# Performance work log

Measured on AMD Instinct MI355X. Metric: run time of the kernel, lower is better.

Reference implementation:

```python
import jax, jax.numpy as jnp
import numpy as np

B, T_DEC, S_ENC, D = 4, 128, 1024, 512
UNITS = 128


def setup_inputs() -> dict:
    key = jax.random.key(0)
    ks = jax.random.split(key, 5)
    dec = jax.random.normal(ks[0], (B, T_DEC, D), dtype=jnp.float32)
    enc = jax.random.normal(ks[1], (B, S_ENC, D), dtype=jnp.float32)
    # Glorot-ish scaled dense params
    W1 = jax.random.normal(ks[2], (D, UNITS), dtype=jnp.float32) / np.sqrt(D)
    b1 = jnp.zeros((UNITS,), dtype=jnp.float32)
    W2 = jax.random.normal(ks[3], (D, UNITS), dtype=jnp.float32) / np.sqrt(D)
    b2 = jnp.zeros((UNITS,), dtype=jnp.float32)
    v = jax.random.normal(ks[4], (UNITS,), dtype=jnp.float32) / np.sqrt(UNITS)
    v_b = jnp.zeros((1,), dtype=jnp.float32)
    return {"decoder_output": dec, "encoder_output": enc,
            "W1": W1, "b1": b1, "W2": W2, "b2": b2, "v": v, "v_b": v_b}


def reference(decoder_output, encoder_output, W1, b1, W2, b2, v, v_b):
    # Hoist the loop-invariant encoder projection (original recomputes it per step).
    w_enc = encoder_output @ W1 + b1            # [B, S, U]
    w_dec = decoder_output @ W2 + b2            # [B, T, U]
    # score[b,t,s] = v . tanh(w_enc[b,s] + w_dec[b,t]) + v_bias
    feat = jnp.tanh(w_enc[:, None, :, :] + w_dec[:, :, None, :])  # [B, T, S, U]
    scores = jnp.einsum('btsu,u->bts', feat, v) + v_b[0]          # [B, T, S]
    attention_weights = jax.nn.softmax(scores, axis=-1)           # [B, T, S]
    context_vector = jnp.einsum('bts,bsd->btd', attention_weights, encoder_output)
    return (context_vector, attention_weights)
```

## Files before the change

kernel.cpp:

```cpp
#include <hip/hip_runtime.h>
#include <math.h>

#define NB 4
#define TD 128
#define SE 1024
#define DD 512
#define UN 128
#define KSPLIT 4
#define SSPLIT 8

__device__ __forceinline__ float exp2_raw(float x) {
  float r;
  asm("v_exp_f32 %0, %1" : "=v"(r) : "v"(x));
  return r;
}

__global__ __launch_bounds__(512, 2) void k_proj(const float* __restrict__ enc,
                                                 const float* __restrict__ dec,
                                                 const float* __restrict__ W1,
                                                 const float* __restrict__ b1,
                                                 const float* __restrict__ W2,
                                                 const float* __restrict__ b2,
                                                 float* __restrict__ wencT,
                                                 float* __restrict__ wdec) {
  __shared__ __align__(16) float At[16 * DD];
  __shared__ float red[KSPLIT][16][129];

  const int tx = threadIdx.x;
  const int rb = blockIdx.x;
  const bool is_enc = rb < 256;
  const int row_base = rb * 16;
  const float* __restrict__ src = is_enc
      ? (enc + (size_t)row_base * DD)
      : (dec + (size_t)(row_base - NB * SE) * DD);
  const float* __restrict__ W = is_enc ? W1 : W2;
  const float* __restrict__ bias = is_enc ? b1 : b2;
  const float K2 = 2.88539008f;

#pragma unroll
  for (int i = 0; i < 4; ++i) {
    const int idx = (i * 512 + tx) * 4;
    *(float4*)&At[idx] = *(const float4*)(src + idx);
  }
  __syncthreads();

  const int u2 = (tx & 63) * 2;
  const int wave = tx >> 6;
  const int ks = wave & 3;
  const int rh = wave >> 2;
  const int kb = ks * 128;
  const float* __restrict__ Wp = W + (size_t)kb * UN + u2;

  float acc[8][2] = {};
  for (int k = 0; k < 128; k += 4) {
    float4 a[8];
#pragma unroll
    for (int r = 0; r < 8; ++r)
      a[r] = *(const float4*)&At[(rh * 8 + r) * DD + kb + k];
#pragma unroll
    for (int j = 0; j < 4; ++j) {
      const float2 w = *(const float2*)(Wp + (size_t)(k + j) * UN);
#pragma unroll
      for (int r = 0; r < 8; ++r) {
        const float arj = ((const float*)&a[r])[j];
        acc[r][0] = fmaf(arj, w.x, acc[r][0]);
        acc[r][1] = fmaf(arj, w.y, acc[r][1]);
      }
    }
  }

#pragma unroll
  for (int r = 0; r < 8; ++r) {
    red[ks][rh * 8 + r][u2]     = acc[r][0];
    red[ks][rh * 8 + r][u2 + 1] = acc[r][1];
  }
  __syncthreads();

  const int u = tx >> 2;
  const int rq = (tx & 3) * 4;
  const float bu = bias[u];
  float o[4];
#pragma unroll
  for (int j = 0; j < 4; ++j) {
    const int row = rq + j;
    const float s = (red[0][row][u] + red[1][row][u]) +
                    (red[2][row][u] + red[3][row][u]);
    o[j] = K2 * (s + bu);
  }
  if (is_enc) {
    const int b = row_base >> 10;
    const int s0 = row_base & 1023;
    *(float4*)(wencT + (size_t)(b * UN + u) * SE + s0 + rq) =
        make_float4(o[0], o[1], o[2], o[3]);
  } else {
    const int rb0 = row_base - NB * SE;
#pragma unroll
    for (int j = 0; j < 4; ++j)
      wdec[(size_t)(rb0 + rq + j) * UN + u] = o[j];
  }
}

__global__ __launch_bounds__(1024, 1) void k_score(const float* __restrict__ wdec,
                                                   const float* __restrict__ v,
                                                   const float* __restrict__ wencT,
                                                   float* __restrict__ attn) {
  __shared__ __align__(16) float wdE[2][UN];
  __shared__ __align__(16) float nv2[UN];
  __shared__ __align__(16) float parts[4][2][SE];
  __shared__ float redM[2][4], redS[2][4];

  const int wg = blockIdx.x;
  const int b = wg >> 6;
  const int t0 = (wg & 63) * 2;
  const int bt0 = b * TD + t0;
  const int tx = threadIdx.x;

  if (tx < 2 * UN) {
    const int tt = tx >> 7, u = tx & 127;
    wdE[tt][u] = exp2_raw(wdec[(size_t)(bt0 + tt) * UN + u]);
    if (tx < UN) nv2[tx] = -2.0f * v[tx];
  }
  __syncthreads();

  const int sq = tx & 255;
  const int uq = tx >> 8;
  const float* wp = wencT + (size_t)(b * UN + uq * 32) * SE + sq * 4;

  float a0[4] = {}, a1[4] = {};
#pragma unroll 4
  for (int ui = 0; ui < 32; ++ui) {
    const int u = uq * 32 + ui;
    const float4 w = *(const float4*)(wp + (size_t)ui * SE);
    const float nvu = nv2[u];
    const float E0 = wdE[0][u];
    const float E1 = wdE[1][u];
#pragma unroll
    for (int j = 0; j < 4; ++j) {
      const float e = exp2_raw(((const float*)&w)[j]);
      const float r0 = __builtin_amdgcn_rcpf(fmaf(e, E0, 1.0f));
      a0[j] = fmaf(nvu, r0, a0[j]);
      const float r1 = __builtin_amdgcn_rcpf(fmaf(e, E1, 1.0f));
      a1[j] = fmaf(nvu, r1, a1[j]);
    }
  }
  *(float4*)&parts[uq][0][sq * 4] = make_float4(a0[0], a0[1], a0[2], a0[3]);
  *(float4*)&parts[uq][1][sq * 4] = make_float4(a1[0], a1[1], a1[2], a1[3]);
  __syncthreads();

  float sc[4], pv[4];
  const int tt = tx >> 8;
  const int q = tx & 255;
  if (tx < 512) {
    const float4 g0 = *(const float4*)&parts[0][tt][q * 4];
    const float4 g1 = *(const float4*)&parts[1][tt][q * 4];
    const float4 g2 = *(const float4*)&parts[2][tt][q * 4];
    const float4 g3 = *(const float4*)&parts[3][tt][q * 4];
    sc[0] = (g0.x + g1.x) + (g2.x + g3.x);
    sc[1] = (g0.y + g1.y) + (g2.y + g3.y);
    sc[2] = (g0.z + g1.z) + (g2.z + g3.z);
    sc[3] = (g0.w + g1.w) + (g2.w + g3.w);
    float m = fmaxf(fmaxf(sc[0], sc[1]), fmaxf(sc[2], sc[3]));
#pragma unroll
    for (int off = 32; off; off >>= 1) m = fmaxf(m, __shfl_xor(m, off));
    if ((tx & 63) == 0) redM[tt][(tx >> 6) & 3] = m;
  }
  __syncthreads();
  if (tx < 512) {
    const float m = fmaxf(fmaxf(redM[tt][0], redM[tt][1]),
                          fmaxf(redM[tt][2], redM[tt][3]));
    float s = 0.f;
#pragma unroll
    for (int j = 0; j < 4; ++j) { pv[j] = __expf(sc[j] - m); s += pv[j]; }
#pragma unroll
    for (int off = 32; off; off >>= 1) s += __shfl_xor(s, off);
    if ((tx & 63) == 0) redS[tt][(tx >> 6) & 3] = s;
  }
  __syncthreads();
  if (tx < 512) {
    const float s = (redS[tt][0] + redS[tt][1]) + (redS[tt][2] + redS[tt][3]);
    const float rinv = 1.0f / s;
    float* arow = attn + (size_t)(bt0 + tt) * SE + q * 4;
    *(float4*)arow = make_float4(pv[0] * rinv, pv[1] * rinv, pv[2] * rinv, pv[3] * rinv);
  }
}

__global__ __launch_bounds__(256, 2) void k_ctx_part(const float* __restrict__ attn,
                                                     const float* __restrict__ enc,
                                                     float* __restrict__ part) {
  __shared__ __align__(16) float at[8][128];
  const int wg = blockIdx.x;
  const int sch = wg & 7;
  const int tg = (wg >> 3) & 15;
  const int b = wg >> 7;
  const int tx = threadIdx.x;
  const int sbeg = sch * 128;
  {
    const int i = tx >> 5, c = (tx & 31) * 4;
    *(float4*)&at[i][c] =
        *(const float4*)(attn + (size_t)(b * TD + tg * 8 + i) * SE + sbeg + c);
  }
  __syncthreads();
  const int d0 = (tx & 127) * 4;
  const int th = tx >> 7;
  const float* ep = enc + ((size_t)b * SE + sbeg) * DD + d0;
  float4 acc[4] = {};
  for (int s = 0; s < 128; ++s) {
    const float4 ev = *(const float4*)(ep + (size_t)s * DD);
#pragma unroll
    for (int i = 0; i < 4; ++i) {
      const float aij = at[th * 4 + i][s];
      acc[i].x = fmaf(aij, ev.x, acc[i].x);
      acc[i].y = fmaf(aij, ev.y, acc[i].y);
      acc[i].z = fmaf(aij, ev.z, acc[i].z);
      acc[i].w = fmaf(aij, ev.w, acc[i].w);
    }
  }
  float* pb = part + ((size_t)sch * (NB * TD) + b * TD + tg * 8 + th * 4) * DD + d0;
#pragma unroll
  for (int i = 0; i < 4; ++i)
    *(float4*)(pb + (size_t)i * DD) = acc[i];
}

__global__ __launch_bounds__(256, 2) void k_red(const float* __restrict__ part,
                                                float* __restrict__ ctx) {
  const size_t N = (size_t)NB * TD * DD;
  const size_t i = ((size_t)blockIdx.x * 256 + threadIdx.x) * 4;
  float4 o = *(const float4*)(part + i);
#pragma unroll
  for (int s = 1; s < SSPLIT; ++s) {
    const float4 q = *(const float4*)(part + (size_t)s * N + i);
    o.x += q.x; o.y += q.y; o.z += q.z; o.w += q.w;
  }
  *(float4*)(ctx + i) = o;
}

extern "C" void kernel_launch(void* const* d_in, const int* in_sizes, int n_in,
                              void* d_out, int out_size, void* d_ws, size_t ws_size,
                              hipStream_t stream) {
  const float* dec = (const float*)d_in[0];
  const float* enc = (const float*)d_in[1];
  const float* W1  = (const float*)d_in[2];
  const float* b1  = (const float*)d_in[3];
  const float* W2  = (const float*)d_in[4];
  const float* b2  = (const float*)d_in[5];
  const float* v   = (const float*)d_in[6];

  float* ctx  = (float*)d_out;
  float* attn = (float*)d_out + (size_t)NB * TD * DD;

  float* ws    = (float*)d_ws;
  float* wencT = ws;
  float* wdec  = wencT + (size_t)NB * UN * SE;
  float* ctxpart = wdec + (size_t)NB * TD * UN;

  hipLaunchKernelGGL(k_proj, dim3(288), dim3(512), 0, stream,
                     enc, dec, W1, b1, W2, b2, wencT, wdec);
  hipLaunchKernelGGL(k_score, dim3(256), dim3(1024), 0, stream,
                     wdec, v, wencT, attn);
  hipLaunchKernelGGL(k_ctx_part, dim3(512), dim3(256), 0, stream, attn, enc, ctxpart);
  hipLaunchKernelGGL(k_red, dim3(256), dim3(256), 0, stream, ctxpart, ctx);
}
```

Before: 52.54 us.

## Fuse split-S context partials and reduction into one kernel via LDS reduction

Replaces the two-kernel context computation (per-S-chunk partial sums written to workspace, then a separate reduction kernel) with a single kernel. Each block covers 8 decoder rows by a 128-wide D slice across all of S. Its 8 waves each handle one S chunk and reduce through shared memory before writing ctx directly. This removes one launch and the global round trip of the partial buffers. The cost is fewer, larger blocks (256 of 512 threads), narrower float2 loads, and more LDS use per block.

```diff
diff --git a/kernel.cpp b/kernel.cpp
--- a/kernel.cpp
+++ b/kernel.cpp
@@ -7,7 +7,6 @@
 #define DD 512
 #define UN 128
 #define KSPLIT 4
-#define SSPLIT 8
 
 __device__ __forceinline__ float exp2_raw(float x) {
   float r;
@@ -184,54 +183,58 @@
   }
 }
 
-__global__ __launch_bounds__(256, 2) void k_ctx_part(const float* __restrict__ attn,
-                                                     const float* __restrict__ enc,
-                                                     float* __restrict__ part) {
-  __shared__ __align__(16) float at[8][128];
+__global__ __launch_bounds__(512, 2) void k_ctx(const float* __restrict__ attn,
+                                                const float* __restrict__ enc,
+                                                float* __restrict__ ctx) {
+  __shared__ __align__(16) float at[8][SE];
+  __shared__ __align__(16) float red[8][8][128];
+
   const int wg = blockIdx.x;
-  const int sch = wg & 7;
-  const int tg = (wg >> 3) & 15;
-  const int b = wg >> 7;
+  const int dt = wg & 3;
+  const int tg = (wg >> 2) & 15;
+  const int b = wg >> 6;
   const int tx = threadIdx.x;
-  const int sbeg = sch * 128;
-  {
-    const int i = tx >> 5, c = (tx & 31) * 4;
-    *(float4*)&at[i][c] =
-        *(const float4*)(attn + (size_t)(b * TD + tg * 8 + i) * SE + sbeg + c);
-  }
-  __syncthreads();
-  const int d0 = (tx & 127) * 4;
-  const int th = tx >> 7;
-  const float* ep = enc + ((size_t)b * SE + sbeg) * DD + d0;
-  float4 acc[4] = {};
+
+#pragma unroll
+  for (int i = 0; i < 4; ++i) {
+    const int idx = i * 512 + tx;
+    const int row = idx >> 8;
+    const int c = (idx & 255) * 4;
+    *(float4*)&at[row][c] =
+        *(const float4*)(attn + (size_t)(b * TD + tg * 8 + row) * SE + c);
+  }
+  __syncthreads();
+
+  const int w = tx >> 6;
+  const int dp = (tx & 63) * 2;
+  const int sbeg = w * 128;
+  const float* ep = enc + ((size_t)b * SE + sbeg) * DD + dt * 128 + dp;
+
+  float2 acc[8] = {};
   for (int s = 0; s < 128; ++s) {
-    const float4 ev = *(const float4*)(ep + (size_t)s * DD);
-#pragma unroll
-    for (int i = 0; i < 4; ++i) {
-      const float aij = at[th * 4 + i][s];
-      acc[i].x = fmaf(aij, ev.x, acc[i].x);
-      acc[i].y = fmaf(aij, ev.y, acc[i].y);
-      acc[i].z = fmaf(aij, ev.z, acc[i].z);
-      acc[i].w = fmaf(aij, ev.w, acc[i].w);
+    const float2 ev = *(const float2*)(ep + (size_t)s * DD);
+#pragma unroll
+    for (int t = 0; t < 8; ++t) {
+      const float a = at[t][sbeg + s];
+      acc[t].x = fmaf(a, ev.x, acc[t].x);
+      acc[t].y = fmaf(a, ev.y, acc[t].y);
     }
   }
-  float* pb = part + ((size_t)sch * (NB * TD) + b * TD + tg * 8 + th * 4) * DD + d0;
-#pragma unroll
-  for (int i = 0; i < 4; ++i)
-    *(float4*)(pb + (size_t)i * DD) = acc[i];
-}
-
-__global__ __launch_bounds__(256, 2) void k_red(const float* __restrict__ part,
-                                                float* __restrict__ ctx) {
-  const size_t N = (size_t)NB * TD * DD;
-  const size_t i = ((size_t)blockIdx.x * 256 + threadIdx.x) * 4;
-  float4 o = *(const float4*)(part + i);
-#pragma unroll
-  for (int s = 1; s < SSPLIT; ++s) {
-    const float4 q = *(const float4*)(part + (size_t)s * N + i);
-    o.x += q.x; o.y += q.y; o.z += q.z; o.w += q.w;
-  }
-  *(float4*)(ctx + i) = o;
+#pragma unroll
+  for (int t = 0; t < 8; ++t)
+    *(float2*)&red[w][t][dp] = acc[t];
+  __syncthreads();
+
+  const int t = tx >> 6;
+  const int d2 = (tx & 63) * 2;
+  float ox = 0.f, oy = 0.f;
+#pragma unroll
+  for (int q = 0; q < 8; ++q) {
+    ox += red[q][t][d2];
+    oy += red[q][t][d2 + 1];
+  }
+  *(float2*)(ctx + (size_t)(b * TD + tg * 8 + t) * DD + dt * 128 + d2) =
+      make_float2(ox, oy);
 }
 
 extern "C" void kernel_launch(void* const* d_in, const int* in_sizes, int n_in,
@@ -251,12 +254,10 @@
   float* ws    = (float*)d_ws;
   float* wencT = ws;
   float* wdec  = wencT + (size_t)NB * UN * SE;
-  float* ctxpart = wdec + (size_t)NB * TD * UN;
 
   hipLaunchKernelGGL(k_proj, dim3(288), dim3(512), 0, stream,
                      enc, dec, W1, b1, W2, b2, wencT, wdec);
   hipLaunchKernelGGL(k_score, dim3(256), dim3(1024), 0, stream,
                      wdec, v, wencT, attn);
-  hipLaunchKernelGGL(k_ctx_part, dim3(512), dim3(256), 0, stream, attn, enc, ctxpart);
-  hipLaunchKernelGGL(k_red, dim3(256), dim3(256), 0, stream, ctxpart, ctx);
-}
+  hipLaunchKernelGGL(k_ctx, dim3(256), dim3(512), 0, stream, attn, enc, ctx);
+}
```

Result: faster. 50.80 us (-3.3%).
